# Kernel optimization log

Measured on AMD Instinct MI355X. Metric: run time of the kernel, lower is better.

Reference implementation:

```python
import jax, jax.numpy as jnp
import numpy as np

B, C, T, D = 16, 1024, 2048, 512
EPS = 1e-5


def setup_inputs() -> dict:
    key = jax.random.key(0)
    ks = jax.random.split(key, 11)
    s_c = 1.0 / np.sqrt(C)
    s_d = 1.0 / np.sqrt(D)
    return {
        "x": jax.random.normal(ks[0], (B, C, T), dtype=jnp.float32),
        "Wq": jax.random.uniform(ks[1], (D, C), jnp.float32, -s_c, s_c),
        "bq": jax.random.uniform(ks[2], (D,), jnp.float32, -s_c, s_c),
        "Wk": jax.random.uniform(ks[3], (D, C), jnp.float32, -s_c, s_c),
        "bk": jax.random.uniform(ks[4], (D,), jnp.float32, -s_c, s_c),
        "Wv": jax.random.uniform(ks[5], (D, C), jnp.float32, -s_c, s_c),
        "bv": jax.random.uniform(ks[6], (D,), jnp.float32, -s_c, s_c),
        "Wo": jax.random.uniform(ks[7], (C, D), jnp.float32, -s_d, s_d),
        "bo": jax.random.uniform(ks[8], (C,), jnp.float32, -s_d, s_d),
        "gamma": jax.random.normal(ks[9], (C,), dtype=jnp.float32) * 0.1,
        "beta": jax.random.normal(ks[10], (C,), dtype=jnp.float32) * 0.1,
    }


def reference(x, Wq, bq, Wk, bk, Wv, bv, Wo, bo, gamma, beta):
    b, c, t = x.shape
    d = Wq.shape[0]
    # 1x1 Conv1d projections == channel-wise GEMMs
    q = jnp.einsum('dc,bct->btd', Wq, x) + bq            # (B, T, D)
    k = jnp.einsum('dc,bct->bdt', Wk, x) + bk[None, :, None]  # (B, D, T)
    v = jnp.einsum('dc,bct->bdt', Wv, x) + bv[None, :, None]  # (B, D, T)
    # sub_sample: MaxPool1d(kernel=2) on key/value along time
    k = k.reshape(b, d, t // 2, 2).max(axis=-1)          # (B, D, S)
    v = v.reshape(b, d, t // 2, 2).max(axis=-1)          # (B, D, S)
    # softmax-free attention: (Q @ K) / T then @ V
    attn = jnp.einsum('btd,bds->bts', q, k) / t          # (B, T, S)
    out = jnp.einsum('bts,bds->bdt', attn, v)            # (B, D, T)
    # output 1x1 conv
    y = jnp.einsum('cd,bdt->bct', Wo, out) + bo[None, :, None]  # (B, C, T)
    # BatchNorm1d (training-mode batch stats, biased variance)
    mu = y.mean(axis=(0, 2), keepdims=True)
    var = y.var(axis=(0, 2), keepdims=True)
    y = gamma[None, :, None] * (y - mu) * jax.lax.rsqrt(var + EPS) + beta[None, :, None]
    return y + x
```

## Files before the change

kernel.cpp:

```cpp
#include <hip/hip_runtime.h>

typedef unsigned short ushort_t;
typedef __bf16 bf16x8 __attribute__((ext_vector_type(8)));
typedef float floatx4 __attribute__((ext_vector_type(4)));
typedef ushort_t ushortx8 __attribute__((ext_vector_type(8)));

__device__ __forceinline__ ushort_t f2bf(float f) {
  union { float f; unsigned int u; } c; c.f = f;
  unsigned int r = c.u + 0x7FFFu + ((c.u >> 16) & 1u);
  return (ushort_t)(r >> 16);
}

__device__ __forceinline__ void async16(const ushort_t* g, ushort_t* l) {
  __builtin_amdgcn_global_load_lds(
      (const __attribute__((address_space(1))) unsigned int*)g,
      (__attribute__((address_space(3))) unsigned int*)l, 16, 0, 0);
}

template<int BIASM, int POOLM, bool OUTF32>
__global__ __launch_bounds__(512, 2)
void gemm256(const ushort_t* __restrict__ A, long aStr,
             const ushort_t* __restrict__ B, long bStr,
             void* __restrict__ Cp, long cStr,
             int K, int lda, int ldb, int ldc,
             const float* __restrict__ bias, float scale)
{
  __shared__ ushort_t As[2][256][64];
  __shared__ ushort_t Bs[2][256][64];

  A += (long)blockIdx.z * aStr;
  B += (long)blockIdx.z * bStr;
  float* Cf = (float*)Cp + (OUTF32 ? (long)blockIdx.z * cStr : 0);
  ushort_t* Cb = (ushort_t*)Cp + (OUTF32 ? 0 : (long)blockIdx.z * cStr);
  const int m0 = blockIdx.y * 256;
  const int n0 = blockIdx.x * 256;
  const int tid = threadIdx.x;
  const int lane = tid & 63;
  const int wid = tid >> 6;
  const int wm = wid >> 2;
  const int wn = wid & 3;
  const int l15 = lane & 15;
  const int lq  = lane >> 4;

  const int srow = tid >> 3;
  const int scb  = (((tid & 7) ^ (srow & 7)) << 3);
  const int dcb  = (tid & 7) << 3;

  const ushort_t* gA = A + (long)(m0 + srow) * lda + scb;
  const ushort_t* gB = B + (long)(n0 + srow) * ldb + scb;

  const int pb0 = ((lq ^ (l15 & 7)) << 3);
  const int pb1 = (((4 | lq) ^ (l15 & 7)) << 3);

  floatx4 acc[8][4];
#pragma unroll
  for (int i = 0; i < 8; ++i)
#pragma unroll
    for (int j = 0; j < 4; ++j)
#pragma unroll
      for (int r = 0; r < 4; ++r) acc[i][j][r] = 0.0f;

  bf16x8 aA[4][2], bB0[2][2], bB1[2][2];

  const int NT = K >> 6;
  const int NI = NT >> 1;

#define STAGE_A(sl, hf, kt) do { \
    const ushort_t* _s = gA + (long)((hf) * 128) * lda + ((kt) << 6); \
    async16(_s,                  &As[sl][(hf)*128      + srow][dcb]); \
    async16(_s + (long)64 * lda, &As[sl][(hf)*128 + 64 + srow][dcb]); \
  } while (0)
#define STAGE_B(sl, hf, kt) do { \
    const ushort_t* _s = gB + (long)((hf) * 128) * ldb + ((kt) << 6); \
    async16(_s,                  &Bs[sl][(hf)*128      + srow][dcb]); \
    async16(_s + (long)64 * ldb, &Bs[sl][(hf)*128 + 64 + srow][dcb]); \
  } while (0)
#define LD_A(sl, mh) do { \
    _Pragma("unroll") for (int _i = 0; _i < 4; ++_i) { \
      const int _r = wm*128 + (mh)*64 + _i*16 + l15; \
      aA[_i][0] = *(const bf16x8*)&As[sl][_r][pb0]; \
      aA[_i][1] = *(const bf16x8*)&As[sl][_r][pb1]; } \
  } while (0)
#define LD_B(sl, nh, dst) do { \
    _Pragma("unroll") for (int _j = 0; _j < 2; ++_j) { \
      const int _r = wn*64 + (nh)*32 + _j*16 + l15; \
      dst[_j][0] = *(const bf16x8*)&Bs[sl][_r][pb0]; \
      dst[_j][1] = *(const bf16x8*)&Bs[sl][_r][pb1]; } \
  } while (0)
#define MMA(mh, nh, bfr) do { \
    __builtin_amdgcn_s_setprio(1); \
    _Pragma("unroll") for (int _i = 0; _i < 4; ++_i) \
    _Pragma("unroll") for (int _j = 0; _j < 2; ++_j) { \
      floatx4& _c = acc[(mh)*4 + _i][(nh)*2 + _j]; \
      _c = __builtin_amdgcn_mfma_f32_16x16x32_bf16(aA[_i][0], (bfr)[_j][0], _c, 0, 0, 0); \
      _c = __builtin_amdgcn_mfma_f32_16x16x32_bf16(aA[_i][1], (bfr)[_j][1], _c, 0, 0, 0); } \
    __builtin_amdgcn_s_setprio(0); \
  } while (0)
#define SBAR  __builtin_amdgcn_s_barrier()
#define LGKM0 asm volatile("s_waitcnt lgkmcnt(0)" ::: "memory")
#define VM4   asm volatile("s_waitcnt vmcnt(4)" ::: "memory")
#define VM0   asm volatile("s_waitcnt vmcnt(0)" ::: "memory")

  STAGE_A(0, 0, 0); STAGE_A(0, 1, 0); STAGE_B(0, 0, 0); STAGE_B(0, 1, 0);
  STAGE_A(1, 0, 1); STAGE_B(1, 1, 1);
  VM4; SBAR;

  for (int i = 0; i < NI - 1; ++i) {
    const int t1 = 2*i + 1, t2 = 2*i + 2, t3 = 2*i + 3;
    LD_A(0, 0); LD_B(0, 0, bB0); STAGE_A(1, 1, t1);
    SBAR; LGKM0; MMA(0, 0, bB0); SBAR;
    LD_B(0, 1, bB1); STAGE_B(1, 0, t1);
    SBAR; LGKM0; MMA(0, 1, bB1); SBAR;
    LD_A(0, 1); STAGE_A(0, 0, t2);
    SBAR; LGKM0; MMA(1, 1, bB1); SBAR;
    STAGE_B(0, 1, t2);
    SBAR; LGKM0; MMA(1, 0, bB0); VM4; SBAR;
    LD_A(1, 0); LD_B(1, 0, bB0); STAGE_A(0, 1, t2);
    SBAR; LGKM0; MMA(0, 0, bB0); SBAR;
    LD_B(1, 1, bB1); STAGE_B(0, 0, t2);
    SBAR; LGKM0; MMA(0, 1, bB1); SBAR;
    LD_A(1, 1); STAGE_A(1, 0, t3);
    SBAR; LGKM0; MMA(1, 1, bB1); SBAR;
    STAGE_B(1, 1, t3);
    SBAR; LGKM0; MMA(1, 0, bB0); VM4; SBAR;
  }
  {
    const int t1 = NT - 1;
    LD_A(0, 0); LD_B(0, 0, bB0); STAGE_A(1, 1, t1);
    SBAR; LGKM0; MMA(0, 0, bB0); SBAR;
    LD_B(0, 1, bB1); STAGE_B(1, 0, t1);
    SBAR; LGKM0; MMA(0, 1, bB1); SBAR;
    LD_A(0, 1);
    SBAR; LGKM0; MMA(1, 1, bB1); SBAR;
    SBAR; LGKM0; MMA(1, 0, bB0); VM0; SBAR;
    LD_A(1, 0); LD_B(1, 0, bB0);
    SBAR; LGKM0; MMA(0, 0, bB0); SBAR;
    LD_B(1, 1, bB1);
    SBAR; LGKM0; MMA(0, 1, bB1); SBAR;
    LD_A(1, 1);
    SBAR; LGKM0; MMA(1, 1, bB1); SBAR;
    LGKM0; MMA(1, 0, bB0);
  }
#undef STAGE_A
#undef STAGE_B
#undef LD_A
#undef LD_B
#undef MMA
#undef SBAR
#undef LGKM0
#undef VM4
#undef VM0

#pragma unroll
  for (int mi = 0; mi < 8; ++mi) {
    const int mbase = m0 + wm*128 + (mi >> 2)*64 + (mi & 3)*16 + lq*4;
#pragma unroll
    for (int nj = 0; nj < 4; ++nj) {
      const int n = n0 + wn*64 + (nj >> 1)*32 + (nj & 1)*16 + l15;
      float v[4];
#pragma unroll
      for (int r = 0; r < 4; ++r) {
        v[r] = acc[mi][nj][r] * scale;
        if (BIASM == 1) v[r] += bias[mbase + r];
      }
      if (BIASM == 2) {
        const float bn_ = bias[n];
#pragma unroll
        for (int r = 0; r < 4; ++r) v[r] += bn_;
      }
      if (POOLM == 0) {
#pragma unroll
        for (int r = 0; r < 4; ++r) {
          if (OUTF32) Cf[(long)(mbase + r) * ldc + n] = v[r];
          else        Cb[(long)(mbase + r) * ldc + n] = f2bf(v[r]);
        }
      } else if (POOLM == 1) {
#pragma unroll
        for (int r = 0; r < 4; ++r) {
          float o = __shfl_xor(v[r], 1);
          float w = fmaxf(v[r], o);
          if ((lane & 1) == 0) {
            if (OUTF32) Cf[(long)(mbase + r) * ldc + (n >> 1)] = w;
            else        Cb[(long)(mbase + r) * ldc + (n >> 1)] = f2bf(w);
          }
        }
      } else {
        float w0 = fmaxf(v[0], v[1]);
        float w1 = fmaxf(v[2], v[3]);
        const int mh = mbase >> 1;
        if (OUTF32) {
          Cf[(long)mh * ldc + n] = w0;
          Cf[(long)(mh + 1) * ldc + n] = w1;
        } else {
          Cb[(long)mh * ldc + n] = f2bf(w0);
          Cb[(long)(mh + 1) * ldc + n] = f2bf(w1);
        }
      }
    }
  }
}

__global__ __launch_bounds__(256)
void transpose_f32_bf16(const float* __restrict__ src, ushort_t* __restrict__ dst,
                        int Rr, int Cl)
{
  __shared__ ushort_t tileT[64][72];
  const long boff = (long)blockIdx.z * Rr * Cl;
  const int t0 = blockIdx.x * 64;
  const int r0 = blockIdx.y * 64;
  const int tx = threadIdx.x & 15;
  const int ty = threadIdx.x >> 4;
#pragma unroll
  for (int i = 0; i < 4; ++i) {
    const int c = ty + 16 * i;
    floatx4 v = *(const floatx4*)&src[boff + (long)(r0 + c) * Cl + t0 + 4 * tx];
#pragma unroll
    for (int j = 0; j < 4; ++j) tileT[4 * tx + j][c] = f2bf(v[j]);
  }
  __syncthreads();
  const int cx = threadIdx.x & 7;
  const int tw = threadIdx.x >> 3;
#pragma unroll
  for (int i = 0; i < 2; ++i) {
    const int t = tw + 32 * i;
    ushortx8 w = *(const ushortx8*)&tileT[t][8 * cx];
    *(ushortx8*)&dst[boff + (long)(t0 + t) * Rr + r0 + 8 * cx] = w;
  }
}

__global__ __launch_bounds__(256)
void convert4(const float* __restrict__ a, const float* __restrict__ b,
              const float* __restrict__ c, const float* __restrict__ d,
              ushort_t* __restrict__ dst, int n)
{
  const float* srcs[4] = {a, b, c, d};
  const float* s = srcs[blockIdx.y];
  int i = blockIdx.x * 256 + threadIdx.x;
  if (i < n) dst[(long)blockIdx.y * n + i] = f2bf(s[i]);
}

__global__ __launch_bounds__(256)
void bn_stats(const float* __restrict__ y, float* __restrict__ stats)
{
  const int c = blockIdx.x;
  float s = 0.0f, s2 = 0.0f;
  for (int b = 0; b < 16; ++b) {
    const floatx4* row = (const floatx4*)(y + ((long)b * 1024 + c) * 2048);
    for (int t = threadIdx.x; t < 512; t += 256) {
      floatx4 v = row[t];
#pragma unroll
      for (int r = 0; r < 4; ++r) { s += v[r]; s2 += v[r] * v[r]; }
    }
  }
#pragma unroll
  for (int o = 32; o > 0; o >>= 1) { s += __shfl_down(s, o); s2 += __shfl_down(s2, o); }
  __shared__ float red[8];
  const int lane = threadIdx.x & 63, w = threadIdx.x >> 6;
  if (lane == 0) { red[w] = s; red[4 + w] = s2; }
  __syncthreads();
  if (threadIdx.x == 0) {
    s = red[0] + red[1] + red[2] + red[3];
    s2 = red[4] + red[5] + red[6] + red[7];
    const float inv = 1.0f / (16.0f * 2048.0f);
    float mean = s * inv;
    float var = s2 * inv - mean * mean;
    stats[c * 2] = mean;
    stats[c * 2 + 1] = rsqrtf(var + 1e-5f);
  }
}

__global__ __launch_bounds__(256)
void bn_apply(float* __restrict__ y, const float* __restrict__ x,
              const float* __restrict__ stats, const float* __restrict__ gamma,
              const float* __restrict__ beta)
{
  const int bc = blockIdx.x;
  const int c = bc & 1023;
  const long off = (long)bc * 2048;
  const float mean = stats[c * 2], rstd = stats[c * 2 + 1];
  const float g = gamma[c] * rstd;
  const float bt = beta[c];
  floatx4* yp = (floatx4*)(y + off);
  const floatx4* xp = (const floatx4*)(x + off);
  for (int t = threadIdx.x; t < 512; t += 256) {
    floatx4 v = yp[t];
    floatx4 xv = xp[t];
#pragma unroll
    for (int r = 0; r < 4; ++r) v[r] = (v[r] - mean) * g + bt + xv[r];
    yp[t] = v;
  }
}

extern "C" void kernel_launch(void* const* d_in, const int* in_sizes, int n_in,
                              void* d_out, int out_size, void* d_ws, size_t ws_size,
                              hipStream_t stream) {
  (void)in_sizes; (void)n_in; (void)out_size; (void)ws_size;
  const float* x  = (const float*)d_in[0];
  const float* Wq = (const float*)d_in[1];
  const float* bq = (const float*)d_in[2];
  const float* Wk = (const float*)d_in[3];
  const float* bk = (const float*)d_in[4];
  const float* Wv = (const float*)d_in[5];
  const float* bv = (const float*)d_in[6];
  const float* Wo = (const float*)d_in[7];
  const float* bo = (const float*)d_in[8];
  const float* gamma = (const float*)d_in[9];
  const float* beta  = (const float*)d_in[10];
  float* out = (float*)d_out;

  const int Cc = 1024, T = 2048, D = 512, S = 1024;

  ushort_t* ws   = (ushort_t*)d_ws;
  ushort_t* xT   = ws;
  ushort_t* Qt   = ws + 33554432;
  ushort_t* Kd   = ws + 50331648;
  ushort_t* V    = ws + 58720256;
  ushort_t* Wt   = ws + 67108864;
  ushort_t* out2 = ws + 71303168;
  ushort_t* Wq_b = ws + 88080384;
  ushort_t* Wk_b = ws + 88604672;
  ushort_t* Wv_b = ws + 89128960;
  ushort_t* Wo_b = ws + 89653248;
  float*    stats = (float*)(ws + 90177536);

  dim3 blk(256);
  dim3 blk512(512);

  convert4<<<dim3(2048, 4), blk, 0, stream>>>(Wq, Wk, Wv, Wo, Wq_b, D * Cc);

  transpose_f32_bf16<<<dim3(T / 64, Cc / 64, 16), blk, 0, stream>>>(x, xT, Cc, T);

  gemm256<2, 0, false><<<dim3(D / 256, T / 256, 16), blk512, 0, stream>>>(
      xT, (long)T * Cc, Wq_b, 0, Qt, (long)T * D, Cc, Cc, Cc, D, bq, 1.0f);
  gemm256<1, 1, false><<<dim3(T / 256, D / 256, 16), blk512, 0, stream>>>(
      Wk_b, 0, xT, (long)T * Cc, Kd, (long)D * S, Cc, Cc, Cc, S, bk, 1.0f);
  gemm256<1, 1, false><<<dim3(T / 256, D / 256, 16), blk512, 0, stream>>>(
      Wv_b, 0, xT, (long)T * Cc, V, (long)D * S, Cc, Cc, Cc, S, bv, 1.0f);

  gemm256<0, 0, false><<<dim3(D / 256, D / 256, 16), blk512, 0, stream>>>(
      V, (long)D * S, Kd, (long)D * S, Wt, (long)D * D,
      S, S, S, D, nullptr, 1.0f);
  gemm256<0, 0, false><<<dim3(D / 256, T / 256, 16), blk512, 0, stream>>>(
      Qt, (long)T * D, Wt, (long)D * D, out2, (long)T * D,
      D, D, D, D, nullptr, 1.0f / 2048.0f);

  gemm256<1, 0, true><<<dim3(T / 256, Cc / 256, 16), blk512, 0, stream>>>(
      Wo_b, 0, out2, (long)T * D, out, (long)Cc * T, D, D, D, T, bo, 1.0f);

  bn_stats<<<dim3(1024), blk, 0, stream>>>(out, stats);
  bn_apply<<<dim3(16384), blk, 0, stream>>>(out, x, stats, gamma, beta);
}
```

Measured before the change: 554.0 us.

## Reassociate attention with Wo, fuse K/V projections, fold BN stats into GEMM epilogue

The output projection is reassociated so Wo is multiplied into the small per-batch DxD matrix (V·Kᵀ) first. This yields a per-batch CxD weight that is applied directly to Q, which removes the T×D intermediate out2 and one large GEMM. The K and V projections are merged into one launch with a concatenated bias. BatchNorm partial sums are computed in the final GEMM epilogue, so the separate full pass that read y for statistics is gone. The epilogue now does extra shuffles and shared-memory work, and it uses more LDS, which could affect occupancy.

```diff
diff --git a/kernel.cpp b/kernel.cpp
--- a/kernel.cpp
+++ b/kernel.cpp
@@ -17,16 +17,18 @@
       (__attribute__((address_space(3))) unsigned int*)l, 16, 0, 0);
 }
 
-template<int BIASM, int POOLM, bool OUTF32>
+template<int BIASM, int POOLM, bool OUTF32, bool STATS = false>
 __global__ __launch_bounds__(512, 2)
 void gemm256(const ushort_t* __restrict__ A, long aStr,
              const ushort_t* __restrict__ B, long bStr,
              void* __restrict__ Cp, long cStr,
              int K, int lda, int ldb, int ldc,
-             const float* __restrict__ bias, float scale)
+             const float* __restrict__ bias, float scale,
+             float2* __restrict__ pstat = nullptr)
 {
   __shared__ ushort_t As[2][256][64];
   __shared__ ushort_t Bs[2][256][64];
+  __shared__ float2 part[4][256];
 
   A += (long)blockIdx.z * aStr;
   B += (long)blockIdx.z * bStr;
@@ -154,6 +156,11 @@
 #pragma unroll
   for (int mi = 0; mi < 8; ++mi) {
     const int mbase = m0 + wm*128 + (mi >> 2)*64 + (mi & 3)*16 + lq*4;
+    float ss[4], ss2[4];
+    if (STATS) {
+#pragma unroll
+      for (int r = 0; r < 4; ++r) { ss[r] = 0.0f; ss2[r] = 0.0f; }
+    }
 #pragma unroll
     for (int nj = 0; nj < 4; ++nj) {
       const int n = n0 + wn*64 + (nj >> 1)*32 + (nj & 1)*16 + l15;
@@ -167,6 +174,10 @@
         const float bn_ = bias[n];
 #pragma unroll
         for (int r = 0; r < 4; ++r) v[r] += bn_;
+      }
+      if (STATS) {
+#pragma unroll
+        for (int r = 0; r < 4; ++r) { ss[r] += v[r]; ss2[r] += v[r] * v[r]; }
       }
       if (POOLM == 0) {
 #pragma unroll
@@ -197,6 +208,29 @@
         }
       }
     }
+    if (STATS) {
+#pragma unroll
+      for (int o = 1; o < 16; o <<= 1) {
+#pragma unroll
+        for (int r = 0; r < 4; ++r) {
+          ss[r]  += __shfl_xor(ss[r],  o);
+          ss2[r] += __shfl_xor(ss2[r], o);
+        }
+      }
+      if (l15 == 0) {
+        const int chb = wm*128 + (mi >> 2)*64 + (mi & 3)*16 + lq*4;
+#pragma unroll
+        for (int r = 0; r < 4; ++r) part[wn][chb + r] = make_float2(ss[r], ss2[r]);
+      }
+    }
+  }
+  if (STATS) {
+    __syncthreads();
+    if (tid < 256) {
+      float2 p0 = part[0][tid], p1 = part[1][tid], p2 = part[2][tid], p3 = part[3][tid];
+      float2 p = make_float2(p0.x + p1.x + p2.x + p3.x, p0.y + p1.y + p2.y + p3.y);
+      pstat[((long)blockIdx.z * gridDim.x + blockIdx.x) * 1024 + m0 + tid] = p;
+    }
   }
 }
 
@@ -231,36 +265,31 @@
 __global__ __launch_bounds__(256)
 void convert4(const float* __restrict__ a, const float* __restrict__ b,
               const float* __restrict__ c, const float* __restrict__ d,
-              ushort_t* __restrict__ dst, int n)
+              ushort_t* __restrict__ dst, int n,
+              const float* __restrict__ bk, const float* __restrict__ bv,
+              float* __restrict__ bkv)
 {
   const float* srcs[4] = {a, b, c, d};
   const float* s = srcs[blockIdx.y];
   int i = blockIdx.x * 256 + threadIdx.x;
   if (i < n) dst[(long)blockIdx.y * n + i] = f2bf(s[i]);
-}
-
-__global__ __launch_bounds__(256)
-void bn_stats(const float* __restrict__ y, float* __restrict__ stats)
+  if (blockIdx.y == 0 && blockIdx.x == 0) {
+    for (int j = threadIdx.x; j < 1024; j += 256)
+      bkv[j] = (j < 512) ? bk[j] : bv[j - 512];
+  }
+}
+
+__global__ __launch_bounds__(64)
+void bn_finalize(const float2* __restrict__ pstat, float* __restrict__ stats)
 {
   const int c = blockIdx.x;
-  float s = 0.0f, s2 = 0.0f;
-  for (int b = 0; b < 16; ++b) {
-    const floatx4* row = (const floatx4*)(y + ((long)b * 1024 + c) * 2048);
-    for (int t = threadIdx.x; t < 512; t += 256) {
-      floatx4 v = row[t];
-#pragma unroll
-      for (int r = 0; r < 4; ++r) { s += v[r]; s2 += v[r] * v[r]; }
-    }
-  }
+  const int lane = threadIdx.x;
+  float2 a = pstat[(long)lane * 1024 + c];
+  float2 b = pstat[(long)(lane + 64) * 1024 + c];
+  float s = a.x + b.x, s2 = a.y + b.y;
 #pragma unroll
   for (int o = 32; o > 0; o >>= 1) { s += __shfl_down(s, o); s2 += __shfl_down(s2, o); }
-  __shared__ float red[8];
-  const int lane = threadIdx.x & 63, w = threadIdx.x >> 6;
-  if (lane == 0) { red[w] = s; red[4 + w] = s2; }
-  __syncthreads();
-  if (threadIdx.x == 0) {
-    s = red[0] + red[1] + red[2] + red[3];
-    s2 = red[4] + red[5] + red[6] + red[7];
+  if (lane == 0) {
     const float inv = 1.0f / (16.0f * 2048.0f);
     float mean = s * inv;
     float var = s2 * inv - mean * mean;
@@ -313,40 +342,40 @@
   ushort_t* ws   = (ushort_t*)d_ws;
   ushort_t* xT   = ws;
   ushort_t* Qt   = ws + 33554432;
-  ushort_t* Kd   = ws + 50331648;
-  ushort_t* V    = ws + 58720256;
-  ushort_t* Wt   = ws + 67108864;
-  ushort_t* out2 = ws + 71303168;
-  ushort_t* Wq_b = ws + 88080384;
-  ushort_t* Wk_b = ws + 88604672;
-  ushort_t* Wv_b = ws + 89128960;
-  ushort_t* Wo_b = ws + 89653248;
-  float*    stats = (float*)(ws + 90177536);
+  ushort_t* KV   = ws + 50331648;
+  ushort_t* WtT  = ws + 67108864;
+  ushort_t* Wco  = ws + 71303168;
+  ushort_t* Wq_b = ws + 79691776;
+  ushort_t* Wo_b = ws + 79691776 + 3 * 524288;
+  float*    bkv  = (float*)(ws + 81788928);
+  float2*   pstat = (float2*)(ws + 81790976);
+  float*    stats = (float*)(ws + 82315264);
 
   dim3 blk(256);
   dim3 blk512(512);
 
-  convert4<<<dim3(2048, 4), blk, 0, stream>>>(Wq, Wk, Wv, Wo, Wq_b, D * Cc);
+  convert4<<<dim3(2048, 4), blk, 0, stream>>>(Wq, Wk, Wv, Wo, Wq_b, D * Cc,
+                                              bk, bv, bkv);
 
   transpose_f32_bf16<<<dim3(T / 64, Cc / 64, 16), blk, 0, stream>>>(x, xT, Cc, T);
 
   gemm256<2, 0, false><<<dim3(D / 256, T / 256, 16), blk512, 0, stream>>>(
       xT, (long)T * Cc, Wq_b, 0, Qt, (long)T * D, Cc, Cc, Cc, D, bq, 1.0f);
-  gemm256<1, 1, false><<<dim3(T / 256, D / 256, 16), blk512, 0, stream>>>(
-      Wk_b, 0, xT, (long)T * Cc, Kd, (long)D * S, Cc, Cc, Cc, S, bk, 1.0f);
-  gemm256<1, 1, false><<<dim3(T / 256, D / 256, 16), blk512, 0, stream>>>(
-      Wv_b, 0, xT, (long)T * Cc, V, (long)D * S, Cc, Cc, Cc, S, bv, 1.0f);
+  gemm256<1, 1, false><<<dim3(T / 256, 2 * D / 256, 16), blk512, 0, stream>>>(
+      Wq_b + (long)D * Cc, 0, xT, (long)T * Cc, KV, (long)2 * D * S,
+      Cc, Cc, Cc, S, bkv, 1.0f);
 
   gemm256<0, 0, false><<<dim3(D / 256, D / 256, 16), blk512, 0, stream>>>(
-      V, (long)D * S, Kd, (long)D * S, Wt, (long)D * D,
+      KV, (long)2 * D * S, KV + (long)D * S, (long)2 * D * S, WtT, (long)D * D,
       S, S, S, D, nullptr, 1.0f);
-  gemm256<0, 0, false><<<dim3(D / 256, T / 256, 16), blk512, 0, stream>>>(
-      Qt, (long)T * D, Wt, (long)D * D, out2, (long)T * D,
+  gemm256<0, 0, false><<<dim3(D / 256, Cc / 256, 16), blk512, 0, stream>>>(
+      Wo_b, 0, WtT, (long)D * D, Wco, (long)Cc * D,
       D, D, D, D, nullptr, 1.0f / 2048.0f);
 
-  gemm256<1, 0, true><<<dim3(T / 256, Cc / 256, 16), blk512, 0, stream>>>(
-      Wo_b, 0, out2, (long)T * D, out, (long)Cc * T, D, D, D, T, bo, 1.0f);
-
-  bn_stats<<<dim3(1024), blk, 0, stream>>>(out, stats);
+  gemm256<1, 0, true, true><<<dim3(T / 256, Cc / 256, 16), blk512, 0, stream>>>(
+      Wco, (long)Cc * D, Qt, (long)T * D, out, (long)Cc * T,
+      D, D, D, T, bo, 1.0f, pstat);
+
+  bn_finalize<<<dim3(1024), dim3(64), 0, stream>>>(pstat, stats);
   bn_apply<<<dim3(16384), blk, 0, stream>>>(out, x, stats, gamma, beta);
 }
```

After: 535.2 us. 1.04x faster.
